# Performance work log

Measured on AMD Instinct MI355X. Metric: run time of the kernel, lower is better.

The kernel has to match this reference:

```python
import jax, jax.numpy as jnp
import numpy as np

B, V, R, P = 1, 2, 512, 64          # batch, views, rays, samples
H, W, F = 480, 640, 256             # image size, feature channels
NEAR, FAR = 0.7, 1.5
DIN = 3 + 3 + (3 + F)               # cam_point(3) + cam_dir(3) + sampled img(3)+feat(F)


def setup_inputs() -> dict:
    key = jax.random.key(0)
    ks = jax.random.split(key, 8)
    ray_origins = jax.random.normal(ks[0], (B, R, 3)) * 0.05
    d = jax.random.normal(ks[1], (B, R, 3)) * 0.2
    d = d.at[..., 2].set(1.0)                      # forward-facing rays (+z)
    ray_directions = d / jnp.linalg.norm(d, axis=-1, keepdims=True)
    images = jax.random.uniform(ks[2], (B, V, H, W, 3))
    K = jnp.array([[500., 0., 320., 0.],
                   [0., 500., 240., 0.],
                   [0., 0., 1., 0.],
                   [0., 0., 0., 1.]])
    intrinsics = jnp.broadcast_to(K, (B, V, 4, 4))
    E = jnp.stack([jnp.eye(4).at[0, 3].set(0.05 * v) for v in range(V)])  # small per-view baseline
    extrinsics_inv = jnp.broadcast_to(E, (B, V, 4, 4))
    combined_features = jax.random.normal(ks[3], (B, V, H, W, F)) * 0.1
    W1 = jax.random.normal(ks[4], (DIN, 128)) * 0.05
    b1 = jnp.zeros((128,))
    W2 = jax.random.normal(ks[5], (128, 128)) * 0.05
    b2 = jnp.zeros((128,))
    Wr = jax.random.normal(ks[6], (128, 4)) * 0.05
    br = jnp.zeros((4,))
    return dict(ray_origins=ray_origins, ray_directions=ray_directions, images=images,
                intrinsics=intrinsics, extrinsics_inv=extrinsics_inv,
                combined_features=combined_features,
                W1=W1, b1=b1, W2=W2, b2=b2, Wr=Wr, br=br)


def bilinear_sample(grid, xy):
    # grid: (B,V,H,W,C), xy: (B,V,R,P,2) pixel coords (x,y) -> (B,V,R,P,C)
    Hh, Ww = grid.shape[2], grid.shape[3]
    x = jnp.clip(xy[..., 0], 0.0, Ww - 1.0)
    y = jnp.clip(xy[..., 1], 0.0, Hh - 1.0)
    x0 = jnp.floor(x).astype(jnp.int32)
    y0 = jnp.floor(y).astype(jnp.int32)
    x1 = jnp.minimum(x0 + 1, Ww - 1)
    y1 = jnp.minimum(y0 + 1, Hh - 1)
    wx = (x - x0)[..., None]
    wy = (y - y0)[..., None]
    bi = jnp.arange(grid.shape[0])[:, None, None, None]
    vi = jnp.arange(grid.shape[1])[None, :, None, None]
    g = lambda yy, xx: grid[bi, vi, yy, xx]
    return (g(y0, x0) * (1 - wx) * (1 - wy) + g(y0, x1) * wx * (1 - wy)
            + g(y1, x0) * (1 - wx) * wy + g(y1, x1) * wx * wy)


def volumetric_render(zs, density, chroma):
    # zs,density: (B,R,P), chroma: (B,R,P,3)
    dists = zs[..., 1:] - zs[..., :-1]
    dists = jnp.concatenate([dists, dists[..., -1:]], axis=-1)
    alpha = 1.0 - jnp.exp(-density * dists)            # sigma_to_alpha
    t = jnp.cumprod(1.0 - alpha + 1e-10, axis=-1)
    trans = jnp.concatenate([jnp.ones_like(t[..., :1]), t[..., :-1]], axis=-1)  # exclusive cumprod
    weights = alpha * trans
    rgb = jnp.sum(weights[..., None] * chroma, axis=-2)
    depth = jnp.sum(weights * zs, axis=-1)
    return rgb, depth, weights


def reference(ray_origins, ray_directions, images, intrinsics, extrinsics_inv,
              combined_features, W1, b1, W2, b2, Wr, br):
    # sample_along_ray
    zs = jnp.broadcast_to(jnp.linspace(NEAR, FAR, P, dtype=jnp.float32), (B, R, P))
    world = ray_origins[:, :, None, :] + zs[..., None] * ray_directions[:, :, None, :]  # (B,R,P,3)
    world_h = jnp.concatenate([world, jnp.ones_like(world[..., :1])], axis=-1)
    # compute_pixel_in_image_mv
    cam = jnp.einsum('bvij,brpj->bvrpi', extrinsics_inv, world_h)          # (B,V,R,P,4)
    pix = jnp.einsum('bvij,bvrpj->bvrpi', intrinsics, cam)
    xy = pix[..., :2] / (pix[..., 2:3] + 1e-8)
    # get_projection_features_mv: gather normalized image + features jointly
    grid = jnp.concatenate([images * 2.0 - 1.0, combined_features], axis=-1)  # (B,V,H,W,3+F)
    feats = bilinear_sample(grid, xy)                                         # (B,V,R,P,3+F)
    # world_to_camera_direction_vector_mv
    cam_dirs = jnp.einsum('bvij,brj->bvri', extrinsics_inv[..., :3, :3], ray_directions)
    dirs = jnp.broadcast_to(cam_dirs[:, :, :, None, :], (B, V, R, P, 3))
    # embedding MLP (MVResNetMLPNeRFEmbedding surrogate) + RenderReadout(4)
    x = jnp.concatenate([cam[..., :3], dirs, feats], axis=-1)                 # (B,V,R,P,DIN)
    h = jax.nn.relu(jnp.einsum('bvrpd,df->bvrpf', x, W1) + b1)
    h = jax.nn.relu(jnp.einsum('bvrpd,df->bvrpf', h, W2) + b2)
    h = h.mean(axis=1)                                                        # fuse views -> (B,R,P,128)
    out = jnp.einsum('brpd,df->brpf', h, Wr) + br
    chroma = jax.nn.sigmoid(out[..., :3])
    density = jax.nn.relu(out[..., 3])
    rgb, depth, _ = volumetric_render(zs, density, chroma)
    return rgb, depth
```

## Files before the change

kernel.cpp:

```cpp
#include <hip/hip_runtime.h>
#include <math.h>

#define NRAYS 512
#define NSAMP 64
#define IMH 480
#define IMW 640
#define NFEAT 256
#define ZNEAR 0.7f
#define ZFAR 1.5f
#define KU1 288
#define W1LO 36864
#define W2OF 73728
#define W2LO 16384
#define H1S 132
#define STGS 36
#define WROW 40
#define WPLANE 5120
#define WBUF 10240

typedef __attribute__((ext_vector_type(8))) short bf16x8;
typedef __attribute__((ext_vector_type(16))) float f32x16;

__device__ __forceinline__ unsigned short bf16rne(float f) {
    unsigned int u = __builtin_bit_cast(unsigned int, f);
    unsigned int r = (u + 0x7FFFu + ((u >> 16) & 1u)) >> 16;
    return (unsigned short)r;
}
__device__ __forceinline__ float bf16tof(unsigned short h) {
    unsigned int u = ((unsigned int)h) << 16;
    return __builtin_bit_cast(float, u);
}
__device__ __forceinline__ unsigned int packsplit(float v) {
    const unsigned short h = bf16rne(v);
    const unsigned short l = bf16rne(v - bf16tof(h));
    return (((unsigned int)h) << 16) | (unsigned int)l;
}
__device__ __forceinline__ void unpack8(uint4 a, uint4 b, bf16x8& hi, bf16x8& lo) {
    union { bf16x8 v; unsigned short u[8]; } H, L;
    const unsigned int w[8] = {a.x, a.y, a.z, a.w, b.x, b.y, b.z, b.w};
    #pragma unroll
    for (int i = 0; i < 8; ++i) {
        H.u[i] = (unsigned short)(w[i] >> 16);
        L.u[i] = (unsigned short)(w[i] & 0xFFFFu);
    }
    hi = H.v; lo = L.v;
}

__global__ __launch_bounds__(256)
void nerf_prep(const float* __restrict__ W1, const float* __restrict__ W2,
               unsigned short* __restrict__ wsu) {
    const int i = blockIdx.x * 256 + threadIdx.x;
    if (i < 36864) {
        const int n = i / KU1, k = i % KU1;
        float val = 0.0f;
        if (k < 9) val = W1[k * 128 + n];
        else if (k >= 16 && k < 272) val = W1[(k - 7) * 128 + n];
        const unsigned short h = bf16rne(val);
        wsu[n * KU1 + k] = h;
        wsu[W1LO + n * KU1 + k] = bf16rne(val - bf16tof(h));
    } else if (i < 53248) {
        const int j = i - 36864;
        const int n = j >> 7, k = j & 127;
        const float val = W2[k * 128 + n];
        const unsigned short h = bf16rne(val);
        wsu[W2OF + n * 128 + k] = h;
        wsu[W2OF + W2LO + n * 128 + k] = bf16rne(val - bf16tof(h));
    }
}

__global__ __launch_bounds__(512, 2)
void nerf_main(const float* __restrict__ rayo,
               const float* __restrict__ rayd,
               const float* __restrict__ images,
               const float* __restrict__ intr,
               const float* __restrict__ einv,
               const float* __restrict__ feats,
               const float* __restrict__ b1,
               const float* __restrict__ b2,
               const float* __restrict__ Wr,
               const float* __restrict__ br,
               const unsigned short* __restrict__ wsu,
               float* __restrict__ out) {
    __shared__ float s_meta[128][12];
    __shared__ float s_cdir[2][4];
    __shared__ unsigned int h1p[128 * H1S];
    __shared__ unsigned short ldsW[2 * WBUF];
    __shared__ unsigned int xstg[4][2][32 * STGS];
    __shared__ float s_part[2][128][4];

    const int t = threadIdx.x;
    const int r = blockIdx.x;
    const int w8 = __builtin_amdgcn_readfirstlane(t >> 6);
    const int mt = w8 >> 1;
    const int np = w8 & 1;
    const int lane = t & 63;
    const int l31 = lane & 31;
    const int lh = lane >> 5;
    const int sq = lane >> 2;
    const int qq = lane & 3;
    const int vW = w8 >> 2;
    const int rit = np * 16 + sq;
    constexpr float STEP = (ZFAR - ZNEAR) / (NSAMP - 1);

    const int sp = t >> 8;
    const int sn = (t & 255) >> 1;
    const int sh = (t & 1) * 16;

    uint4 wa, wb;
    {
        const unsigned short* s = wsu + sp*W1LO + sn*KU1 + sh;
        wa = *reinterpret_cast<const uint4*>(s);
        wb = *reinterpret_cast<const uint4*>(s + 8);
    }

    if (t < 128) {
        const int vv = t >> 6, p = t & 63;
        const float ox = rayo[r*3+0], oy = rayo[r*3+1], oz = rayo[r*3+2];
        const float dx = rayd[r*3+0], dy = rayd[r*3+1], dz = rayd[r*3+2];
        const float z = ZNEAR + p * STEP;
        const float wxp = ox + z*dx, wyp = oy + z*dy, wzp = oz + z*dz;
        const float* E = einv + vv*16;
        const float cx = E[0]*wxp + E[1]*wyp + E[2]*wzp + E[3];
        const float cy = E[4]*wxp + E[5]*wyp + E[6]*wzp + E[7];
        const float cz = E[8]*wxp + E[9]*wyp + E[10]*wzp + E[11];
        const float cw = E[12]*wxp + E[13]*wyp + E[14]*wzp + E[15];
        const float* Km = intr + vv*16;
        const float px = Km[0]*cx + Km[1]*cy + Km[2]*cz + Km[3]*cw;
        const float py = Km[4]*cx + Km[5]*cy + Km[6]*cz + Km[7]*cw;
        const float pz = Km[8]*cx + Km[9]*cy + Km[10]*cz + Km[11]*cw;
        const float inv = pz + 1e-8f;
        float fx = px / inv, fy = py / inv;
        fx = fminf(fmaxf(fx, 0.0f), (float)(IMW-1));
        fy = fminf(fmaxf(fy, 0.0f), (float)(IMH-1));
        const int x0 = (int)floorf(fx), y0 = (int)floorf(fy);
        const int x1 = min(x0+1, IMW-1), y1 = min(y0+1, IMH-1);
        const int base = vv*IMH*IMW;
        int4 o4; o4.x = (base + y0*IMW + x0) * NFEAT;
                 o4.y = (base + y0*IMW + x1) * NFEAT;
                 o4.z = (base + y1*IMW + x0) * NFEAT;
                 o4.w = (base + y1*IMW + x1) * NFEAT;
        *(int4*)&s_meta[t][0] = o4;
        s_meta[t][4] = fx - (float)x0;
        s_meta[t][5] = fy - (float)y0;
        s_meta[t][6] = cx; s_meta[t][7] = cy; s_meta[t][8] = cz;
        if (p == 0) {
            s_cdir[vv][0] = E[0]*dx + E[1]*dy + E[2]*dz;
            s_cdir[vv][1] = E[4]*dx + E[5]*dy + E[6]*dz;
            s_cdir[vv][2] = E[8]*dx + E[9]*dy + E[10]*dz;
        }
    }
    {
        unsigned short* d = ldsW + sp*WPLANE + sn*WROW + sh;
        *reinterpret_cast<uint4*>(d)     = wa;
        *reinterpret_cast<uint4*>(d + 8) = wb;
    }
    __syncthreads();

    const float* mg = s_meta[w8*16 + sq];
    const int4 og = *(const int4*)mg;
    const float wx = mg[4], wy = mg[5];
    const float w00 = (1.f-wx)*(1.f-wy), w01 = wx*(1.f-wy);
    const float w10 = (1.f-wx)*wy,       w11 = wx*wy;
    const float* t00 = feats + og.x;
    const float* t01 = feats + og.y;
    const float* t10 = feats + og.z;
    const float* t11 = feats + og.w;

    float ia = 0.f, ib = 0.f;
    if (qq == 1 || qq == 2) {
        const int i00 = (og.x >> 8) * 3, i01 = (og.y >> 8) * 3;
        const int i10 = (og.z >> 8) * 3, i11 = (og.w >> 8) * 3;
        if (qq == 1) {
            ia = 2.0f*(w00*images[i00+0] + w01*images[i01+0] + w10*images[i10+0] + w11*images[i11+0]) - 1.0f;
            ib = 2.0f*(w00*images[i00+1] + w01*images[i01+1] + w10*images[i10+1] + w11*images[i11+1]) - 1.0f;
        } else {
            ia = 2.0f*(w00*images[i00+2] + w01*images[i01+2] + w10*images[i10+2] + w11*images[i11+2]) - 1.0f;
        }
    }

    float4 La[4], Lb[4];
    {
        const int f1 = qq*4;
        Lb[0] = *reinterpret_cast<const float4*>(t00 + f1);
        Lb[1] = *reinterpret_cast<const float4*>(t01 + f1);
        Lb[2] = *reinterpret_cast<const float4*>(t10 + f1);
        Lb[3] = *reinterpret_cast<const float4*>(t11 + f1);
    }
    {
        float f0[4], f1[4];
        if (qq == 0)      { f0[0]=mg[6]; f0[1]=mg[7]; f0[2]=mg[8]; f0[3]=s_cdir[vW][0]; }
        else if (qq == 1) { f0[0]=s_cdir[vW][1]; f0[1]=s_cdir[vW][2]; f0[2]=ia; f0[3]=ib; }
        else if (qq == 2) { f0[0]=ia; f0[1]=0.f; f0[2]=0.f; f0[3]=0.f; }
        else              { f0[0]=0.f; f0[1]=0.f; f0[2]=0.f; f0[3]=0.f; }
        f1[0] = w00*Lb[0].x + w01*Lb[1].x + w10*Lb[2].x + w11*Lb[3].x;
        f1[1] = w00*Lb[0].y + w01*Lb[1].y + w10*Lb[2].y + w11*Lb[3].y;
        f1[2] = w00*Lb[0].z + w01*Lb[1].z + w10*Lb[2].z + w11*Lb[3].z;
        f1[3] = w00*Lb[0].w + w01*Lb[1].w + w10*Lb[2].w + w11*Lb[3].w;
        uint4 u0, u1;
        u0.x = packsplit(f0[0]); u0.y = packsplit(f0[1]);
        u0.z = packsplit(f0[2]); u0.w = packsplit(f0[3]);
        u1.x = packsplit(f1[0]); u1.y = packsplit(f1[1]);
        u1.z = packsplit(f1[2]); u1.w = packsplit(f1[3]);
        unsigned int* xw = &xstg[mt][0][rit*STGS];
        *reinterpret_cast<uint4*>(xw + qq*4)      = u0;
        *reinterpret_cast<uint4*>(xw + 16 + qq*4) = u1;
    }
    {
        const int n0 = 16 + qq*4, n1 = 32 + qq*4;
        La[0] = *reinterpret_cast<const float4*>(t00 + n0);
        La[1] = *reinterpret_cast<const float4*>(t01 + n0);
        La[2] = *reinterpret_cast<const float4*>(t10 + n0);
        La[3] = *reinterpret_cast<const float4*>(t11 + n0);
        Lb[0] = *reinterpret_cast<const float4*>(t00 + n1);
        Lb[1] = *reinterpret_cast<const float4*>(t01 + n1);
        Lb[2] = *reinterpret_cast<const float4*>(t10 + n1);
        Lb[3] = *reinterpret_cast<const float4*>(t11 + n1);
    }
    __syncthreads();

    f32x16 acc0, acc1;
    #pragma unroll
    for (int i = 0; i < 16; ++i) { acc0[i] = 0.0f; acc1[i] = 0.0f; }
    const int bn0 = (np*2)*32 + l31;
    int cur = 0;
    #pragma unroll
    for (int kc = 0; kc < 9; ++kc) {
        {
            const unsigned short* s = (kc < 8)
                ? (wsu + sp*W1LO + sn*KU1 + (kc+1)*32 + sh)
                : (wsu + W2OF + sp*W2LO + sn*128 + sh);
            wa = *reinterpret_cast<const uint4*>(s);
            wb = *reinterpret_cast<const uint4*>(s + 8);
        }
        if (kc < 8) {
            const int c = kc + 1;
            float f0[4], f1[4];
            f0[0] = w00*La[0].x + w01*La[1].x + w10*La[2].x + w11*La[3].x;
            f0[1] = w00*La[0].y + w01*La[1].y + w10*La[2].y + w11*La[3].y;
            f0[2] = w00*La[0].z + w01*La[1].z + w10*La[2].z + w11*La[3].z;
            f0[3] = w00*La[0].w + w01*La[1].w + w10*La[2].w + w11*La[3].w;
            if (c == 8) {
                f1[0]=0.f; f1[1]=0.f; f1[2]=0.f; f1[3]=0.f;
            } else {
                f1[0] = w00*Lb[0].x + w01*Lb[1].x + w10*Lb[2].x + w11*Lb[3].x;
                f1[1] = w00*Lb[0].y + w01*Lb[1].y + w10*Lb[2].y + w11*Lb[3].y;
                f1[2] = w00*Lb[0].z + w01*Lb[1].z + w10*Lb[2].z + w11*Lb[3].z;
                f1[3] = w00*Lb[0].w + w01*Lb[1].w + w10*Lb[2].w + w11*Lb[3].w;
            }
            uint4 u0, u1;
            u0.x = packsplit(f0[0]); u0.y = packsplit(f0[1]);
            u0.z = packsplit(f0[2]); u0.w = packsplit(f0[3]);
            u1.x = packsplit(f1[0]); u1.y = packsplit(f1[1]);
            u1.z = packsplit(f1[2]); u1.w = packsplit(f1[3]);
            unsigned int* xw = &xstg[mt][cur^1][rit*STGS];
            *reinterpret_cast<uint4*>(xw + qq*4)      = u0;
            *reinterpret_cast<uint4*>(xw + 16 + qq*4) = u1;
            if (kc < 7) {
                const int n0 = (kc+2)*32 - 16 + qq*4;
                La[0] = *reinterpret_cast<const float4*>(t00 + n0);
                La[1] = *reinterpret_cast<const float4*>(t01 + n0);
                La[2] = *reinterpret_cast<const float4*>(t10 + n0);
                La[3] = *reinterpret_cast<const float4*>(t11 + n0);
                if (kc < 6) {
                    const int n1 = n0 + 16;
                    Lb[0] = *reinterpret_cast<const float4*>(t00 + n1);
                    Lb[1] = *reinterpret_cast<const float4*>(t01 + n1);
                    Lb[2] = *reinterpret_cast<const float4*>(t10 + n1);
                    Lb[3] = *reinterpret_cast<const float4*>(t11 + n1);
                }
            }
        }
        {
            const unsigned int* xb = &xstg[mt][cur][0];
            #pragma unroll
            for (int ks = 0; ks < 2; ++ks) {
                const uint4 ua = *reinterpret_cast<const uint4*>(xb + l31*STGS + ks*16 + lh*8);
                const uint4 ub = *reinterpret_cast<const uint4*>(xb + l31*STGS + ks*16 + lh*8 + 4);
                bf16x8 ah, al;
                unpack8(ua, ub, ah, al);
                const unsigned short* wk = ldsW + cur*WBUF + ks*16 + lh*8;
                {
                    const unsigned short* wp = wk + bn0*WROW;
                    const bf16x8 bh = *(const bf16x8*)(wp);
                    const bf16x8 bl = *(const bf16x8*)(wp + WPLANE);
                    acc0 = __builtin_amdgcn_mfma_f32_32x32x16_bf16(ah, bh, acc0, 0, 0, 0);
                    acc0 = __builtin_amdgcn_mfma_f32_32x32x16_bf16(al, bh, acc0, 0, 0, 0);
                    acc0 = __builtin_amdgcn_mfma_f32_32x32x16_bf16(ah, bl, acc0, 0, 0, 0);
                }
                {
                    const unsigned short* wp = wk + (bn0 + 32)*WROW;
                    const bf16x8 bh = *(const bf16x8*)(wp);
                    const bf16x8 bl = *(const bf16x8*)(wp + WPLANE);
                    acc1 = __builtin_amdgcn_mfma_f32_32x32x16_bf16(ah, bh, acc1, 0, 0, 0);
                    acc1 = __builtin_amdgcn_mfma_f32_32x32x16_bf16(al, bh, acc1, 0, 0, 0);
                    acc1 = __builtin_amdgcn_mfma_f32_32x32x16_bf16(ah, bl, acc1, 0, 0, 0);
                }
            }
        }
        {
            unsigned short* d = ldsW + (cur^1)*WBUF + sp*WPLANE + sn*WROW + sh;
            *reinterpret_cast<uint4*>(d)     = wa;
            *reinterpret_cast<uint4*>(d + 8) = wb;
        }
        __syncthreads();
        cur ^= 1;
    }

    {
        const float b1v0 = b1[bn0], b1v1 = b1[bn0 + 32];
        #pragma unroll
        for (int j = 0; j < 16; ++j) {
            const int row = mt*32 + (j & 3) + 8*(j >> 2) + 4*lh;
            h1p[row*H1S + bn0]      = packsplit(fmaxf(acc0[j] + b1v0, 0.0f));
            h1p[row*H1S + bn0 + 32] = packsplit(fmaxf(acc1[j] + b1v1, 0.0f));
        }
    }
    __syncthreads();

    #pragma unroll
    for (int i = 0; i < 16; ++i) { acc0[i] = 0.0f; acc1[i] = 0.0f; }
    #pragma unroll
    for (int kc = 0; kc < 4; ++kc) {
        if (kc < 3) {
            const unsigned short* s = wsu + W2OF + sp*W2LO + sn*128 + (kc+1)*32 + sh;
            wa = *reinterpret_cast<const uint4*>(s);
            wb = *reinterpret_cast<const uint4*>(s + 8);
        }
        const unsigned int* hb = h1p + (mt*32 + l31)*H1S + kc*32;
        #pragma unroll
        for (int ks = 0; ks < 2; ++ks) {
            const uint4 ua = *reinterpret_cast<const uint4*>(hb + ks*16 + lh*8);
            const uint4 ub = *reinterpret_cast<const uint4*>(hb + ks*16 + lh*8 + 4);
            bf16x8 ah, al;
            unpack8(ua, ub, ah, al);
            const unsigned short* wk = ldsW + cur*WBUF + ks*16 + lh*8;
            {
                const unsigned short* wp = wk + bn0*WROW;
                const bf16x8 bh = *(const bf16x8*)(wp);
                const bf16x8 bl = *(const bf16x8*)(wp + WPLANE);
                acc0 = __builtin_amdgcn_mfma_f32_32x32x16_bf16(ah, bh, acc0, 0, 0, 0);
                acc0 = __builtin_amdgcn_mfma_f32_32x32x16_bf16(al, bh, acc0, 0, 0, 0);
                acc0 = __builtin_amdgcn_mfma_f32_32x32x16_bf16(ah, bl, acc0, 0, 0, 0);
            }
            {
                const unsigned short* wp = wk + (bn0 + 32)*WROW;
                const bf16x8 bh = *(const bf16x8*)(wp);
                const bf16x8 bl = *(const bf16x8*)(wp + WPLANE);
                acc1 = __builtin_amdgcn_mfma_f32_32x32x16_bf16(ah, bh, acc1, 0, 0, 0);
                acc1 = __builtin_amdgcn_mfma_f32_32x32x16_bf16(al, bh, acc1, 0, 0, 0);
                acc1 = __builtin_amdgcn_mfma_f32_32x32x16_bf16(ah, bl, acc1, 0, 0, 0);
            }
        }
        if (kc < 3) {
            unsigned short* d = ldsW + (cur^1)*WBUF + sp*WPLANE + sn*WROW + sh;
            *reinterpret_cast<uint4*>(d)     = wa;
            *reinterpret_cast<uint4*>(d + 8) = wb;
            __syncthreads();
            cur ^= 1;
        }
    }

    {
        const float b2v0 = b2[bn0], b2v1 = b2[bn0 + 32];
        const float4 wr0 = *reinterpret_cast<const float4*>(Wr + bn0*4);
        const float4 wr1 = *reinterpret_cast<const float4*>(Wr + (bn0+32)*4);
        float pr[16][4];
        #pragma unroll
        for (int j = 0; j < 16; ++j) {
            const float h0 = fmaxf(acc0[j] + b2v0, 0.0f);
            const float h1v = fmaxf(acc1[j] + b2v1, 0.0f);
            pr[j][0] = h0*wr0.x + h1v*wr1.x;
            pr[j][1] = h0*wr0.y + h1v*wr1.y;
            pr[j][2] = h0*wr0.z + h1v*wr1.z;
            pr[j][3] = h0*wr0.w + h1v*wr1.w;
        }
        #pragma unroll
        for (int b = 0; b < 4; ++b) {
            const int m = 1 << b;
            const int Sh = 8 >> b;
            const bool hi = (l31 >> b) & 1;
            #pragma unroll
            for (int i = 0; i < 8; ++i) {
                if (i < Sh) {
                    #pragma unroll
                    for (int q = 0; q < 4; ++q) {
                        const float send = hi ? pr[i][q] : pr[Sh + i][q];
                        const float keep = hi ? pr[Sh + i][q] : pr[i][q];
                        const float rcv  = __shfl_xor(send, m, 64);
                        pr[i][q] = keep + rcv;
                    }
                }
            }
        }
        #pragma unroll
        for (int q = 0; q < 4; ++q)
            pr[0][q] += __shfl_xor(pr[0][q], 16, 64);
        if (l31 < 16) {
            const int jf = ((l31 & 1) << 3) | (((l31 >> 1) & 1) << 2)
                         | (((l31 >> 2) & 1) << 1) | ((l31 >> 3) & 1);
            const int row = mt*32 + (jf & 3) + 8*(jf >> 2) + 4*lh;
            float4 o;
            o.x = pr[0][0]; o.y = pr[0][1]; o.z = pr[0][2]; o.w = pr[0][3];
            *reinterpret_cast<float4*>(&s_part[np][row][0]) = o;
        }
    }
    __syncthreads();

    if (t < NSAMP) {
        const int p = t;
        const float o0 = 0.5f*((s_part[0][p][0] + s_part[1][p][0]) + (s_part[0][64+p][0] + s_part[1][64+p][0])) + br[0];
        const float o1 = 0.5f*((s_part[0][p][1] + s_part[1][p][1]) + (s_part[0][64+p][1] + s_part[1][64+p][1])) + br[1];
        const float o2 = 0.5f*((s_part[0][p][2] + s_part[1][p][2]) + (s_part[0][64+p][2] + s_part[1][64+p][2])) + br[2];
        const float o3 = 0.5f*((s_part[0][p][3] + s_part[1][p][3]) + (s_part[0][64+p][3] + s_part[1][64+p][3])) + br[3];
        const float c0 = 1.0f/(1.0f + __expf(-o0));
        const float c1 = 1.0f/(1.0f + __expf(-o1));
        const float c2 = 1.0f/(1.0f + __expf(-o2));
        const float dens = fmaxf(o3, 0.0f);
        const float zp = ZNEAR + p * STEP;
        const float zn = ZNEAR + (p+1) * STEP;
        const float dlast = (ZNEAR + 63*STEP) - (ZNEAR + 62*STEP);
        const float dist = (p == NSAMP-1) ? dlast : (zn - zp);
        const float alpha = 1.0f - __expf(-dens*dist);
        float scan = 1.0f - alpha + 1e-10f;
        #pragma unroll
        for (int off = 1; off < 64; off <<= 1) {
            const float vsh = __shfl_up(scan, off, 64);
            if (p >= off) scan *= vsh;
        }
        float trans = __shfl_up(scan, 1, 64);
        if (p == 0) trans = 1.0f;
        const float w = alpha * trans;
        float s0 = w*c0, s1 = w*c1, s2 = w*c2, sd = w*zp;
        #pragma unroll
        for (int m = 32; m > 0; m >>= 1) {
            s0 += __shfl_xor(s0, m, 64);
            s1 += __shfl_xor(s1, m, 64);
            s2 += __shfl_xor(s2, m, 64);
            sd += __shfl_xor(sd, m, 64);
        }
        if (p == 0) {
            out[r*3+0] = s0; out[r*3+1] = s1; out[r*3+2] = s2;
            out[NRAYS*3 + r] = sd;
        }
    }
}

extern "C" void kernel_launch(void* const* d_in, const int* in_sizes, int n_in,
                              void* d_out, int out_size, void* d_ws, size_t ws_size,
                              hipStream_t stream) {
    const float* rayo   = (const float*)d_in[0];
    const float* rayd   = (const float*)d_in[1];
    const float* images = (const float*)d_in[2];
    const float* intr   = (const float*)d_in[3];
    const float* einv   = (const float*)d_in[4];
    const float* feats  = (const float*)d_in[5];
    const float* W1     = (const float*)d_in[6];
    const float* b1     = (const float*)d_in[7];
    const float* W2     = (const float*)d_in[8];
    const float* b2     = (const float*)d_in[9];
    const float* Wr     = (const float*)d_in[10];
    const float* br     = (const float*)d_in[11];
    float* out = (float*)d_out;
    unsigned short* wsu = (unsigned short*)d_ws;

    hipLaunchKernelGGL(nerf_prep, dim3(208), dim3(256), 0, stream, W1, W2, wsu);
    hipLaunchKernelGGL(nerf_main, dim3(NRAYS), dim3(512), 0, stream,
                       rayo, rayd, images, intr, einv, feats, b1, b2, Wr, br, wsu, out);
}
```

Baseline: 50.45 us.

## Pack shared memory into aliased buffer, swizzle weight tiles, read W2 from global

Replaces the separate shared arrays with one byte buffer in which h1p aliases the meta, staging and weight regions. Weight rows shrink from 40 to 32 elements, with an XOR swizzle to avoid bank conflicts. Layer-2 weights are now read straight from global memory/L2 instead of being double-buffered through LDS, which removes three barriers. Launch bounds rise from 2 to 4 blocks per CU to get more occupancy, at the cost of tighter register limits and uncoalesced global weight reads in layer 2.

```diff
diff --git a/kernel.cpp b/kernel.cpp
--- a/kernel.cpp
+++ b/kernel.cpp
@@ -14,9 +14,16 @@
 #define W2LO 16384
 #define H1S 132
 #define STGS 36
-#define WROW 40
-#define WPLANE 5120
-#define WBUF 10240
+#define WROW 32
+#define WPLANE 4096
+#define WBUF 8192
+#define META_OFF 0
+#define CDIR_OFF 6144
+#define XSTG_OFF 6176
+#define LDSW_OFF 43040
+#define H1_OFF   0
+#define PART_OFF 67584
+#define SMEM_BYTES 75808
 
 typedef __attribute__((ext_vector_type(8))) short bf16x8;
 typedef __attribute__((ext_vector_type(16))) float f32x16;
@@ -68,7 +75,7 @@
     }
 }
 
-__global__ __launch_bounds__(512, 2)
+__global__ __launch_bounds__(512, 4)
 void nerf_main(const float* __restrict__ rayo,
                const float* __restrict__ rayd,
                const float* __restrict__ images,
@@ -81,12 +88,13 @@
                const float* __restrict__ br,
                const unsigned short* __restrict__ wsu,
                float* __restrict__ out) {
-    __shared__ float s_meta[128][12];
-    __shared__ float s_cdir[2][4];
-    __shared__ unsigned int h1p[128 * H1S];
-    __shared__ unsigned short ldsW[2 * WBUF];
-    __shared__ unsigned int xstg[4][2][32 * STGS];
-    __shared__ float s_part[2][128][4];
+    __shared__ __align__(16) unsigned char smem[SMEM_BYTES];
+    float (*s_meta)[12]      = (float(*)[12])(smem + META_OFF);
+    float (*s_cdir)[4]       = (float(*)[4])(smem + CDIR_OFF);
+    unsigned int* xstg       = (unsigned int*)(smem + XSTG_OFF);
+    unsigned short* ldsW     = (unsigned short*)(smem + LDSW_OFF);
+    unsigned int* h1p        = (unsigned int*)(smem + H1_OFF);
+    float (*s_part)[128][4]  = (float(*)[128][4])(smem + PART_OFF);
 
     const int t = threadIdx.x;
     const int r = blockIdx.x;
@@ -105,6 +113,8 @@
     const int sp = t >> 8;
     const int sn = (t & 255) >> 1;
     const int sh = (t & 1) * 16;
+    const int ssw = (sn >> 1) & 3;
+    const int sc0 = sh >> 3;
 
     uint4 wa, wb;
     {
@@ -150,9 +160,9 @@
         }
     }
     {
-        unsigned short* d = ldsW + sp*WPLANE + sn*WROW + sh;
-        *reinterpret_cast<uint4*>(d)     = wa;
-        *reinterpret_cast<uint4*>(d + 8) = wb;
+        unsigned short* dbase = ldsW + sp*WPLANE + sn*WROW;
+        *reinterpret_cast<uint4*>(dbase + ((sc0 ^ ssw) << 3))       = wa;
+        *reinterpret_cast<uint4*>(dbase + (((sc0+1) ^ ssw) << 3))   = wb;
     }
     __syncthreads();
 
@@ -201,7 +211,7 @@
         u0.z = packsplit(f0[2]); u0.w = packsplit(f0[3]);
         u1.x = packsplit(f1[0]); u1.y = packsplit(f1[1]);
         u1.z = packsplit(f1[2]); u1.w = packsplit(f1[3]);
-        unsigned int* xw = &xstg[mt][0][rit*STGS];
+        unsigned int* xw = xstg + (mt*2 + 0)*(32*STGS) + rit*STGS;
         *reinterpret_cast<uint4*>(xw + qq*4)      = u0;
         *reinterpret_cast<uint4*>(xw + 16 + qq*4) = u1;
     }
@@ -221,14 +231,13 @@
     f32x16 acc0, acc1;
     #pragma unroll
     for (int i = 0; i < 16; ++i) { acc0[i] = 0.0f; acc1[i] = 0.0f; }
-    const int bn0 = (np*2)*32 + l31;
+    const int bn0 = np*64 + l31;
+    const int bsw = (bn0 >> 1) & 3;
     int cur = 0;
     #pragma unroll
     for (int kc = 0; kc < 9; ++kc) {
-        {
-            const unsigned short* s = (kc < 8)
-                ? (wsu + sp*W1LO + sn*KU1 + (kc+1)*32 + sh)
-                : (wsu + W2OF + sp*W2LO + sn*128 + sh);
+        if (kc < 8) {
+            const unsigned short* s = wsu + sp*W1LO + sn*KU1 + (kc+1)*32 + sh;
             wa = *reinterpret_cast<const uint4*>(s);
             wb = *reinterpret_cast<const uint4*>(s + 8);
         }
@@ -252,7 +261,7 @@
             u0.z = packsplit(f0[2]); u0.w = packsplit(f0[3]);
             u1.x = packsplit(f1[0]); u1.y = packsplit(f1[1]);
             u1.z = packsplit(f1[2]); u1.w = packsplit(f1[3]);
-            unsigned int* xw = &xstg[mt][cur^1][rit*STGS];
+            unsigned int* xw = xstg + (mt*2 + (cur^1))*(32*STGS) + rit*STGS;
             *reinterpret_cast<uint4*>(xw + qq*4)      = u0;
             *reinterpret_cast<uint4*>(xw + 16 + qq*4) = u1;
             if (kc < 7) {
@@ -271,16 +280,17 @@
             }
         }
         {
-            const unsigned int* xb = &xstg[mt][cur][0];
+            const unsigned int* xb = xstg + (mt*2 + cur)*(32*STGS);
             #pragma unroll
             for (int ks = 0; ks < 2; ++ks) {
                 const uint4 ua = *reinterpret_cast<const uint4*>(xb + l31*STGS + ks*16 + lh*8);
                 const uint4 ub = *reinterpret_cast<const uint4*>(xb + l31*STGS + ks*16 + lh*8 + 4);
                 bf16x8 ah, al;
                 unpack8(ua, ub, ah, al);
-                const unsigned short* wk = ldsW + cur*WBUF + ks*16 + lh*8;
+                const int coff = (((ks*2 + lh) ^ bsw) << 3);
+                const unsigned short* wk = ldsW + cur*WBUF;
                 {
-                    const unsigned short* wp = wk + bn0*WROW;
+                    const unsigned short* wp = wk + bn0*WROW + coff;
                     const bf16x8 bh = *(const bf16x8*)(wp);
                     const bf16x8 bl = *(const bf16x8*)(wp + WPLANE);
                     acc0 = __builtin_amdgcn_mfma_f32_32x32x16_bf16(ah, bh, acc0, 0, 0, 0);
@@ -288,7 +298,7 @@
                     acc0 = __builtin_amdgcn_mfma_f32_32x32x16_bf16(ah, bl, acc0, 0, 0, 0);
                 }
                 {
-                    const unsigned short* wp = wk + (bn0 + 32)*WROW;
+                    const unsigned short* wp = wk + (bn0 + 32)*WROW + coff;
                     const bf16x8 bh = *(const bf16x8*)(wp);
                     const bf16x8 bl = *(const bf16x8*)(wp + WPLANE);
                     acc1 = __builtin_amdgcn_mfma_f32_32x32x16_bf16(ah, bh, acc1, 0, 0, 0);
@@ -297,10 +307,10 @@
                 }
             }
         }
-        {
-            unsigned short* d = ldsW + (cur^1)*WBUF + sp*WPLANE + sn*WROW + sh;
-            *reinterpret_cast<uint4*>(d)     = wa;
-            *reinterpret_cast<uint4*>(d + 8) = wb;
+        if (kc < 8) {
+            unsigned short* dbase = ldsW + (cur^1)*WBUF + sp*WPLANE + sn*WROW;
+            *reinterpret_cast<uint4*>(dbase + ((sc0 ^ ssw) << 3))     = wa;
+            *reinterpret_cast<uint4*>(dbase + (((sc0+1) ^ ssw) << 3)) = wb;
         }
         __syncthreads();
         cur ^= 1;
@@ -319,46 +329,39 @@
 
     #pragma unroll
     for (int i = 0; i < 16; ++i) { acc0[i] = 0.0f; acc1[i] = 0.0f; }
-    #pragma unroll
-    for (int kc = 0; kc < 4; ++kc) {
-        if (kc < 3) {
-            const unsigned short* s = wsu + W2OF + sp*W2LO + sn*128 + (kc+1)*32 + sh;
-            wa = *reinterpret_cast<const uint4*>(s);
-            wb = *reinterpret_cast<const uint4*>(s + 8);
-        }
-        const unsigned int* hb = h1p + (mt*32 + l31)*H1S + kc*32;
-        #pragma unroll
-        for (int ks = 0; ks < 2; ++ks) {
-            const uint4 ua = *reinterpret_cast<const uint4*>(hb + ks*16 + lh*8);
-            const uint4 ub = *reinterpret_cast<const uint4*>(hb + ks*16 + lh*8 + 4);
-            bf16x8 ah, al;
-            unpack8(ua, ub, ah, al);
-            const unsigned short* wk = ldsW + cur*WBUF + ks*16 + lh*8;
-            {
-                const unsigned short* wp = wk + bn0*WROW;
-                const bf16x8 bh = *(const bf16x8*)(wp);
-                const bf16x8 bl = *(const bf16x8*)(wp + WPLANE);
-                acc0 = __builtin_amdgcn_mfma_f32_32x32x16_bf16(ah, bh, acc0, 0, 0, 0);
-                acc0 = __builtin_amdgcn_mfma_f32_32x32x16_bf16(al, bh, acc0, 0, 0, 0);
-                acc0 = __builtin_amdgcn_mfma_f32_32x32x16_bf16(ah, bl, acc0, 0, 0, 0);
+    {
+        const unsigned short* w2b0 = wsu + W2OF + bn0*128 + lh*8;
+        const unsigned short* w2b1 = wsu + W2OF + (bn0+32)*128 + lh*8;
+        const unsigned int* hb = h1p + (mt*32 + l31)*H1S;
+        #pragma unroll
+        for (int kc = 0; kc < 4; ++kc) {
+            #pragma unroll
+            for (int ks = 0; ks < 2; ++ks) {
+                const uint4 ua = *reinterpret_cast<const uint4*>(hb + kc*32 + ks*16 + lh*8);
+                const uint4 ub = *reinterpret_cast<const uint4*>(hb + kc*32 + ks*16 + lh*8 + 4);
+                bf16x8 ah, al;
+                unpack8(ua, ub, ah, al);
+                const int ko = kc*32 + ks*16;
+                {
+                    const unsigned short* wp = w2b0 + ko;
+                    const bf16x8 bh = *(const bf16x8*)(wp);
+                    const bf16x8 bl = *(const bf16x8*)(wp + W2LO);
+                    acc0 = __builtin_amdgcn_mfma_f32_32x32x16_bf16(ah, bh, acc0, 0, 0, 0);
+                    acc0 = __builtin_amdgcn_mfma_f32_32x32x16_bf16(al, bh, acc0, 0, 0, 0);
+                    acc0 = __builtin_amdgcn_mfma_f32_32x32x16_bf16(ah, bl, acc0, 0, 0, 0);
+                }
+                {
+                    const unsigned short* wp = w2b1 + ko;
+                    const bf16x8 bh = *(const bf16x8*)(wp);
+                    const bf16x8 bl = *(const bf16x8*)(wp + W2LO);
+                    acc1 = __builtin_amdgcn_mfma_f32_32x32x16_bf16(ah, bh, acc1, 0, 0, 0);
+                    acc1 = __builtin_amdgcn_mfma_f32_32x32x16_bf16(al, bh, acc1, 0, 0, 0);
+                    acc1 = __builtin_amdgcn_mfma_f32_32x32x16_bf16(ah, bl, acc1, 0, 0, 0);
+                }
             }
-            {
-                const unsigned short* wp = wk + (bn0 + 32)*WROW;
-                const bf16x8 bh = *(const bf16x8*)(wp);
-                const bf16x8 bl = *(const bf16x8*)(wp + WPLANE);
-                acc1 = __builtin_amdgcn_mfma_f32_32x32x16_bf16(ah, bh, acc1, 0, 0, 0);
-                acc1 = __builtin_amdgcn_mfma_f32_32x32x16_bf16(al, bh, acc1, 0, 0, 0);
-                acc1 = __builtin_amdgcn_mfma_f32_32x32x16_bf16(ah, bl, acc1, 0, 0, 0);
-            }
-        }
-        if (kc < 3) {
-            unsigned short* d = ldsW + (cur^1)*WBUF + sp*WPLANE + sn*WROW + sh;
-            *reinterpret_cast<uint4*>(d)     = wa;
-            *reinterpret_cast<uint4*>(d + 8) = wb;
-            __syncthreads();
-            cur ^= 1;
-        }
-    }
+        }
+    }
+    __syncthreads();
 
     {
         const float b2v0 = b2[bn0], b2v1 = b2[bn0 + 32];
```

Result: no change. 50.70 us (+0.5%).
